# Kernel tuning notes

Measured on AMD Instinct MI355X. Metric: run time of the kernel, lower is better.

## Reference

```python
import jax, jax.numpy as jnp
import numpy as np

B, D, N, K, T = 8192, 256, 2048, 512, 8
M_MARGIN = 1.0
LAMBDA_ORTHO = 1e-3
EPS = 1e-10


def _l2(a, b):
    # squared L2 distance along last axis
    return jnp.sum((a - b) ** 2, axis=-1)


def setup_inputs() -> dict:
    key = jax.random.key(0)
    k1, k2, k3, k4, k5 = jax.random.split(key, 5)
    return {
        "v": jax.random.normal(k1, (B, D), dtype=jnp.float32),
        "vhat": jax.random.normal(k2, (B, D), dtype=jnp.float32),
        "g": jax.random.uniform(k3, (B, K), dtype=jnp.float32),
        "F": jax.random.normal(k4, (K, D), dtype=jnp.float32),
        "negatives": jax.random.normal(k5, (N, D), dtype=jnp.float32),
        "mask": jnp.ones((B,), dtype=bool),
    }


def reference(v, vhat, g, F, negatives, mask):
    maskf = mask.astype(v.dtype)
    msum = maskf.sum()

    # ---- contrastive loss (vectorized over the N-negatives loop) ----
    true_dist = _l2(vhat, v)                                   # [B]
    neg_dist = _l2(vhat[:, None, :], negatives[None, :, :])    # [B, N]
    per = jnp.maximum(1.0 + true_dist[:, None] - neg_dist, 0.0)
    ju_per = per.mean(axis=1) * maskf                          # [B]
    Ju = jnp.where(msum == 0, 0.0, ju_per.sum() / msum)

    # ---- focal triplet loss (topk smallest g, gather F rows) ----
    _, idx = jax.lax.top_k(-g, T)                              # [B, T] indices of t smallest
    g_tz = jnp.take_along_axis(g, idx, axis=1)                 # [B, T]
    F_t = F[idx]                                               # [B, T, D]
    g_t = g_tz / (g_tz.sum(axis=1, keepdims=True) + EPS)
    m_t = M_MARGIN * (1.0 - g_t) ** 2                          # [B, T]
    d_neg = _l2(vhat[:, None, :], F_t)                         # [B, T]
    cur = jnp.maximum(m_t + true_dist[:, None] - d_neg, 0.0)
    jt_per = cur.sum(axis=1) * maskf
    Jt = jnp.where(msum == 0, 0.0, jt_per.sum() / msum)

    # ---- orthogonality regularizer: ||F F^T - I||_F, then squared ----
    gram = F @ F.T - jnp.eye(K, dtype=F.dtype)
    ortho = jnp.sqrt(jnp.sum(gram ** 2))

    Jz = Ju + Jt + LAMBDA_ORTHO * ortho ** 2
    return Jz
```

## Files before the change

### kernel.cpp

```cpp
#include <hip/hip_runtime.h>

#define B_N 8192
#define D_N 256
#define N_N 2048
#define K_N 512
#define T_N 8

using short8  = __attribute__((ext_vector_type(8))) short;
using floatx4 = __attribute__((ext_vector_type(4))) float;


__device__ __forceinline__ float wave_reduce_sum(float x) {
  #pragma unroll
  for (int off = 32; off > 0; off >>= 1) x += __shfl_down(x, off, 64);
  return x;
}

__device__ __forceinline__ unsigned int f2bf(float x) {
  unsigned u = __float_as_uint(x);
  return (u + 0x7fffu + ((u >> 16) & 1u)) >> 16;
}

__device__ __forceinline__ unsigned int pack2bf(float x, float y) {
  return f2bf(x) | (f2bf(y) << 16);
}

__device__ __forceinline__ void gload16(const unsigned short* g, unsigned short* l) {
  __builtin_amdgcn_global_load_lds(
      (const __attribute__((address_space(1))) unsigned int*)g,
      (__attribute__((address_space(3))) unsigned int*)l, 16, 0, 0);
}

#define CSWAP(a, b)                                              \
  {                                                              \
    bool sw_ = sv[a] > sv[b];                                    \
    float tv_ = sw_ ? sv[a] : sv[b];                             \
    sv[a] = sw_ ? sv[b] : sv[a];                                 \
    sv[b] = tv_;                                                 \
    int ti_ = sw_ ? si[a] : si[b];                               \
    si[a] = sw_ ? si[b] : si[a];                                 \
    si[b] = ti_;                                                 \
  }

__global__ __launch_bounds__(256) void prep_kernel(
    const float* __restrict__ v, const float* __restrict__ vhat,
    const float* __restrict__ neg, const float* __restrict__ F,
    const float* __restrict__ g,
    unsigned short* __restrict__ vhat_bf, unsigned short* __restrict__ neg_bf,
    unsigned short* __restrict__ F_bf,
    float* __restrict__ td, float* __restrict__ vn2, float* __restrict__ cb,
    float* __restrict__ nn2, float* __restrict__ fn2,
    float* __restrict__ selc, int* __restrict__ seli) {
  int lane = threadIdx.x & 63;
  int row = (blockIdx.x << 2) + (threadIdx.x >> 6);
  if (row < B_N) {
    const float4 a = *(const float4*)(vhat + (size_t)row * D_N + lane * 4);
    const float4 b = *(const float4*)(v + (size_t)row * D_N + lane * 4);
    float dx = a.x - b.x, dy = a.y - b.y, dz = a.z - b.z, dw = a.w - b.w;
    float t = dx * dx + dy * dy + dz * dz + dw * dw;
    float n = a.x * a.x + a.y * a.y + a.z * a.z + a.w * a.w;
    uint2 p;
    p.x = pack2bf(a.x, a.y);
    p.y = pack2bf(a.z, a.w);
    *(uint2*)(vhat_bf + (size_t)row * D_N + lane * 4) = p;
    t = wave_reduce_sum(t);
    n = wave_reduce_sum(n);
    if (lane == 0) {
      td[row] = t;
      vn2[row] = n;
      cb[row] = 1.0f + t - n;
    }
    const float* grow = g + (size_t)row * K_N;
    float sv[8];
    int si[8];
    {
      float4 g0 = *(const float4*)(grow + lane * 8);
      float4 g1 = *(const float4*)(grow + lane * 8 + 4);
      sv[0] = g0.x; sv[1] = g0.y; sv[2] = g0.z; sv[3] = g0.w;
      sv[4] = g1.x; sv[5] = g1.y; sv[6] = g1.z; sv[7] = g1.w;
      #pragma unroll
      for (int j = 0; j < 8; ++j) si[j] = lane * 8 + j;
    }
    CSWAP(0,1) CSWAP(2,3) CSWAP(4,5) CSWAP(6,7)
    CSWAP(0,2) CSWAP(1,3) CSWAP(4,6) CSWAP(5,7)
    CSWAP(1,2) CSWAP(5,6)
    CSWAP(0,4) CSWAP(1,5) CSWAP(2,6) CSWAP(3,7)
    CSWAP(2,4) CSWAP(3,5)
    CSWAP(1,2) CSWAP(3,4) CSWAP(5,6)
    #pragma unroll
    for (int rr = 0; rr < 6; ++rr) {
      const int msk = 1 << rr;
      float pv[8];
      int pi[8];
      #pragma unroll
      for (int j = 0; j < 8; ++j) {
        pv[j] = __shfl_xor(sv[j], msk, 64);
        pi[j] = __shfl_xor(si[j], msk, 64);
      }
      float cv[8];
      int ci[8];
      #pragma unroll
      for (int j = 0; j < 8; ++j) {
        bool mine = sv[j] <= pv[7 - j];
        cv[j] = mine ? sv[j] : pv[7 - j];
        ci[j] = mine ? si[j] : pi[7 - j];
      }
      #pragma unroll
      for (int j = 0; j < 8; ++j) { sv[j] = cv[j]; si[j] = ci[j]; }
      CSWAP(0,4) CSWAP(1,5) CSWAP(2,6) CSWAP(3,7)
      CSWAP(0,2) CSWAP(1,3) CSWAP(4,6) CSWAP(5,7)
      CSWAP(0,1) CSWAP(2,3) CSWAP(4,5) CSWAP(6,7)
    }
    float gsum = 1e-10f;
    #pragma unroll
    for (int t8 = 0; t8 < T_N; ++t8) gsum += sv[t8];
    if (lane == 0) {
      float base = t - n;
      #pragma unroll
      for (int t8 = 0; t8 < T_N; ++t8) {
        float gt = sv[t8] / gsum;
        float mt = (1.0f - gt) * (1.0f - gt);
        selc[(size_t)row * T_N + t8] = mt + base;
        seli[(size_t)row * T_N + t8] = si[t8];
      }
    }
  } else if (row < B_N + N_N) {
    int r = row - B_N;
    const float4 a = *(const float4*)(neg + (size_t)r * D_N + lane * 4);
    float n = a.x * a.x + a.y * a.y + a.z * a.z + a.w * a.w;
    uint2 p;
    p.x = pack2bf(a.x, a.y);
    p.y = pack2bf(a.z, a.w);
    *(uint2*)(neg_bf + (size_t)r * D_N + lane * 4) = p;
    n = wave_reduce_sum(n);
    if (lane == 0) nn2[r] = n;
  } else {
    int r = row - (B_N + N_N);
    const float4 a = *(const float4*)(F + (size_t)r * D_N + lane * 4);
    float n = a.x * a.x + a.y * a.y + a.z * a.z + a.w * a.w;
    uint2 p;
    p.x = pack2bf(a.x, a.y);
    p.y = pack2bf(a.z, a.w);
    *(uint2*)(F_bf + (size_t)r * D_N + lane * 4) = p;
    n = wave_reduce_sum(n);
    if (lane == 0) fn2[r] = n;
  }
}

__global__ __launch_bounds__(256) void main_kernel(
    const unsigned short* __restrict__ vhat_bf, const unsigned short* __restrict__ neg_bf,
    const unsigned short* __restrict__ F_bf,
    const float* __restrict__ cb, const float* __restrict__ nn2,
    const float* __restrict__ fn2, const int* __restrict__ mask,
    float* __restrict__ ju_part, float* __restrict__ or_part,
    float* __restrict__ W) {
  __shared__ __align__(16) unsigned char smem[16384];
  const int bx = blockIdx.x;
  const int tid = threadIdx.x;
  const int lane = tid & 63;
  const int wave = tid >> 6;

  unsigned short* AsU = (unsigned short*)smem;
  unsigned short* BsU = AsU + 4096;
  int r0, c0;
  const unsigned short *Abase, *Bbase;
  int seg;
  if (bx < 1024) {
    seg = 0;
    r0 = (bx >> 4) * 128;
    c0 = (bx & 15) * 128;
    Abase = vhat_bf;
    Bbase = neg_bf;
  } else if (bx < 1040) {
    seg = 1;
    int o = bx - 1024;
    r0 = (o >> 2) * 128;
    c0 = (o & 3) * 128;
    Abase = F_bf;
    Bbase = F_bf;
  } else {
    seg = 2;
    int o = bx - 1040;
    r0 = (o >> 2) * 128;
    c0 = (o & 3) * 128;
    Abase = vhat_bf;
    Bbase = F_bf;
  }
  const int wx = wave & 1, wy = wave >> 1;

  const int c_slot = lane & 3;
  const int rA0 = wave * 32 + (lane >> 2);
  const int rA1 = rA0 + 16;
  const int cg0 = c_slot ^ ((rA0 >> 1) & 3);
  const int cg1 = c_slot ^ ((rA1 >> 1) & 3);
  const unsigned short* gA0 = Abase + (size_t)(r0 + rA0) * D_N + cg0 * 8;
  const unsigned short* gA1 = Abase + (size_t)(r0 + rA1) * D_N + cg1 * 8;
  const unsigned short* gB0 = Bbase + (size_t)(c0 + rA0) * D_N + cg0 * 8;
  const unsigned short* gB1 = Bbase + (size_t)(c0 + rA1) * D_N + cg1 * 8;
  unsigned short* lA0 = AsU + wave * 1024 + lane * 8;
  unsigned short* lA1 = lA0 + 512;
  unsigned short* lB0 = BsU + wave * 1024 + lane * 8;
  unsigned short* lB1 = lB0 + 512;

  const int fr = lane & 15;
  const int fc = lane >> 4;
  int aoff[4], boff[4];
  #pragma unroll
  for (int i = 0; i < 4; ++i) {
    int ra = wy * 64 + i * 16 + fr;
    aoff[i] = ra * 32 + (fc ^ ((ra >> 1) & 3)) * 8;
    int rb = wx * 64 + i * 16 + fr;
    boff[i] = rb * 32 + (fc ^ ((rb >> 1) & 3)) * 8;
  }

  floatx4 acc[4][4];
  #pragma unroll
  for (int i = 0; i < 4; ++i)
    #pragma unroll
    for (int j = 0; j < 4; ++j)
      acc[i][j] = floatx4{0.0f, 0.0f, 0.0f, 0.0f};

  for (int k0 = 0; k0 < D_N; k0 += 32) {
    __syncthreads();
    gload16(gA0 + k0, lA0);
    gload16(gA1 + k0, lA1);
    gload16(gB0 + k0, lB0);
    gload16(gB1 + k0, lB1);
    __syncthreads();
    short8 af[4], bf[4];
    #pragma unroll
    for (int i = 0; i < 4; ++i) af[i] = *(const short8*)(AsU + aoff[i]);
    #pragma unroll
    for (int j = 0; j < 4; ++j) bf[j] = *(const short8*)(BsU + boff[j]);
    #pragma unroll
    for (int i = 0; i < 4; ++i)
      #pragma unroll
      for (int j = 0; j < 4; ++j)
        acc[i][j] = __builtin_amdgcn_mfma_f32_16x16x32_bf16(af[i], bf[j], acc[i][j], 0, 0, 0);
  }

  if (seg == 0) {
    float nns[4];
    #pragma unroll
    for (int j = 0; j < 4; ++j)
      nns[j] = nn2[c0 + wx * 64 + j * 16 + (lane & 15)];
    float lsum = 0.0f;
    #pragma unroll
    for (int i = 0; i < 4; ++i) {
      #pragma unroll
      for (int r = 0; r < 4; ++r) {
        int b = r0 + wy * 64 + i * 16 + (lane >> 4) * 4 + r;
        float cbb = cb[b];
        float mf = (mask[b] != 0) ? 1.0f : 0.0f;
        float rs = 0.0f;
        #pragma unroll
        for (int j = 0; j < 4; ++j) {
          float val = cbb + 2.0f * acc[i][j][r] - nns[j];
          rs += fmaxf(val, 0.0f);
        }
        lsum += mf * rs;
      }
    }
    lsum = wave_reduce_sum(lsum);
    if (lane == 0) ju_part[bx * 4 + wave] = lsum;
  } else if (seg == 1) {
    float lsum = 0.0f;
    #pragma unroll
    for (int i = 0; i < 4; ++i) {
      #pragma unroll
      for (int r = 0; r < 4; ++r) {
        int gi = r0 + wy * 64 + i * 16 + (lane >> 4) * 4 + r;
        #pragma unroll
        for (int j = 0; j < 4; ++j) {
          int gj = c0 + wx * 64 + j * 16 + (lane & 15);
          float s = (gi == gj) ? (fn2[gi] - 1.0f) : acc[i][j][r];
          lsum += s * s;
        }
      }
    }
    lsum = wave_reduce_sum(lsum);
    if (lane == 0) or_part[(bx - 1024) * 4 + wave] = lsum;
  } else {
    #pragma unroll
    for (int i = 0; i < 4; ++i) {
      #pragma unroll
      for (int r = 0; r < 4; ++r) {
        int row = r0 + wy * 64 + i * 16 + (lane >> 4) * 4 + r;
        #pragma unroll
        for (int j = 0; j < 4; ++j) {
          int col = c0 + wx * 64 + j * 16 + (lane & 15);
          W[(size_t)row * K_N + col] = acc[i][j][r];
        }
      }
    }
  }
}

__global__ __launch_bounds__(256) void jt_gather_kernel(
    const int* __restrict__ seli, const float* __restrict__ selc,
    const float* __restrict__ W, const float* __restrict__ fn2,
    const int* __restrict__ mask, float* __restrict__ jt_part) {
  int b = blockIdx.x * 256 + threadIdx.x;
  int4 i0 = *(const int4*)(seli + (size_t)b * 8);
  int4 i1 = *(const int4*)(seli + (size_t)b * 8 + 4);
  float4 c0 = *(const float4*)(selc + (size_t)b * 8);
  float4 c1 = *(const float4*)(selc + (size_t)b * 8 + 4);
  const float* wrow = W + (size_t)b * K_N;
  float s = 0.0f;
  s += fmaxf(c0.x + 2.0f * wrow[i0.x] - fn2[i0.x], 0.0f);
  s += fmaxf(c0.y + 2.0f * wrow[i0.y] - fn2[i0.y], 0.0f);
  s += fmaxf(c0.z + 2.0f * wrow[i0.z] - fn2[i0.z], 0.0f);
  s += fmaxf(c0.w + 2.0f * wrow[i0.w] - fn2[i0.w], 0.0f);
  s += fmaxf(c1.x + 2.0f * wrow[i1.x] - fn2[i1.x], 0.0f);
  s += fmaxf(c1.y + 2.0f * wrow[i1.y] - fn2[i1.y], 0.0f);
  s += fmaxf(c1.z + 2.0f * wrow[i1.z] - fn2[i1.z], 0.0f);
  s += fmaxf(c1.w + 2.0f * wrow[i1.w] - fn2[i1.w], 0.0f);
  s *= (mask[b] != 0) ? 1.0f : 0.0f;
  s = wave_reduce_sum(s);
  __shared__ float red[4];
  if ((threadIdx.x & 63) == 0) red[threadIdx.x >> 6] = s;
  __syncthreads();
  if (threadIdx.x == 0)
    jt_part[blockIdx.x] = red[0] + red[1] + red[2] + red[3];
}

__global__ __launch_bounds__(256) void finalize_kernel(
    const float* __restrict__ jt_part, const float* __restrict__ ju_part,
    const float* __restrict__ or_part, const int* __restrict__ mask,
    float* __restrict__ out) {
  int tid = threadIdx.x;
  float sjt = 0.0f, sju = 0.0f, sor = 0.0f, sm = 0.0f;
  for (int i = tid; i < B_N; i += 256) sm += (mask[i] != 0) ? 1.0f : 0.0f;
  for (int i = tid; i < 4096; i += 256) sju += ju_part[i];
  if (tid < 64) sor = or_part[tid];
  if (tid < 32) sjt = jt_part[tid];
  sjt = wave_reduce_sum(sjt);
  sju = wave_reduce_sum(sju);
  sor = wave_reduce_sum(sor);
  sm  = wave_reduce_sum(sm);
  __shared__ float red[4][4];
  int lane = tid & 63, w = tid >> 6;
  if (lane == 0) {
    red[w][0] = sjt; red[w][1] = sju; red[w][2] = sor; red[w][3] = sm;
  }
  __syncthreads();
  if (tid == 0) {
    float jt = red[0][0] + red[1][0] + red[2][0] + red[3][0];
    float ju = red[0][1] + red[1][1] + red[2][1] + red[3][1];
    float oo = red[0][2] + red[1][2] + red[2][2] + red[3][2];
    float ms = red[0][3] + red[1][3] + red[2][3] + red[3][3];
    float Ju = (ms == 0.0f) ? 0.0f : ju / ((float)N_N * ms);
    float Jt = (ms == 0.0f) ? 0.0f : jt / ms;
    out[0] = Ju + Jt + 1.0e-3f * oo;
  }
}

extern "C" void kernel_launch(void* const* d_in, const int* in_sizes, int n_in,
                              void* d_out, int out_size, void* d_ws, size_t ws_size,
                              hipStream_t stream) {
  (void)in_sizes; (void)n_in; (void)out_size; (void)ws_size;
  const float* v    = (const float*)d_in[0];
  const float* vhat = (const float*)d_in[1];
  const float* g    = (const float*)d_in[2];
  const float* F    = (const float*)d_in[3];
  const float* neg  = (const float*)d_in[4];
  const int*   mask = (const int*)d_in[5];

  float* ws = (float*)d_ws;
  float* W       = ws;
  float* td      = ws + 4194304;
  float* vn2     = ws + 4202496;
  float* cb      = ws + 4210688;
  float* nn2     = ws + 4218880;
  float* fn2     = ws + 4220928;
  float* ju_part = ws + 4221440;
  float* or_part = ws + 4225536;
  float* jt_part = ws + 4225600;
  float* selc    = ws + 4225632;
  int*   seli    = (int*)(ws + 4291168);
  unsigned short* vhat_bf = (unsigned short*)(ws + 4356704);
  unsigned short* neg_bf  = vhat_bf + (size_t)B_N * D_N;
  unsigned short* F_bf    = neg_bf + (size_t)N_N * D_N;

  prep_kernel<<<(B_N + N_N + K_N) / 4, 256, 0, stream>>>(
      v, vhat, neg, F, g, vhat_bf, neg_bf, F_bf, td, vn2, cb, nn2, fn2,
      selc, seli);
  main_kernel<<<1024 + 16 + 256, 256, 0, stream>>>(
      vhat_bf, neg_bf, F_bf, cb, nn2, fn2, mask, ju_part, or_part, W);
  jt_gather_kernel<<<B_N / 256, 256, 0, stream>>>(
      seli, selc, W, fn2, mask, jt_part);
  finalize_kernel<<<1, 256, 0, stream>>>(jt_part, ju_part, or_part, mask,
                                         (float*)d_out);
}
```

Measured before the change: 126.3 us.

## Fuse focal-triplet gather into GEMM epilogue, drop W matrix round-trip

The vhat·F^T GEMM blocks no longer write the full 8192x512 fp32 W matrix to global memory. Each block stages 16-row slices of its accumulator tile in shared memory and evaluates the hinge terms for the selected top-k indices that fall in its column range, writing per-wave partial sums. This removes a 16 MB write and a separate gather kernel launch. The cost is extra __syncthreads in the epilogue and a larger partial-sum array for the finalize kernel to reduce.

```diff
diff --git a/kernel.cpp b/kernel.cpp
--- a/kernel.cpp
+++ b/kernel.cpp
@@ -152,8 +152,9 @@
     const unsigned short* __restrict__ F_bf,
     const float* __restrict__ cb, const float* __restrict__ nn2,
     const float* __restrict__ fn2, const int* __restrict__ mask,
+    const float* __restrict__ selc, const int* __restrict__ seli,
     float* __restrict__ ju_part, float* __restrict__ or_part,
-    float* __restrict__ W) {
+    float* __restrict__ jt_part) {
   __shared__ __align__(16) unsigned char smem[16384];
   const int bx = blockIdx.x;
   const int tid = threadIdx.x;
@@ -281,47 +282,35 @@
     lsum = wave_reduce_sum(lsum);
     if (lane == 0) or_part[(bx - 1024) * 4 + wave] = lsum;
   } else {
+    float* Wt = (float*)smem;
+    const int quad = lane >> 4, col15 = lane & 15;
+    const int rl = tid >> 3;
+    const int t8 = tid & 7;
+    float jts = 0.0f;
     #pragma unroll
     for (int i = 0; i < 4; ++i) {
+      __syncthreads();
       #pragma unroll
       for (int r = 0; r < 4; ++r) {
-        int row = r0 + wy * 64 + i * 16 + (lane >> 4) * 4 + r;
+        int row_local = wy * 16 + quad * 4 + r;
         #pragma unroll
-        for (int j = 0; j < 4; ++j) {
-          int col = c0 + wx * 64 + j * 16 + (lane & 15);
-          W[(size_t)row * K_N + col] = acc[i][j][r];
-        }
-      }
-    }
-  }
-}
-
-__global__ __launch_bounds__(256) void jt_gather_kernel(
-    const int* __restrict__ seli, const float* __restrict__ selc,
-    const float* __restrict__ W, const float* __restrict__ fn2,
-    const int* __restrict__ mask, float* __restrict__ jt_part) {
-  int b = blockIdx.x * 256 + threadIdx.x;
-  int4 i0 = *(const int4*)(seli + (size_t)b * 8);
-  int4 i1 = *(const int4*)(seli + (size_t)b * 8 + 4);
-  float4 c0 = *(const float4*)(selc + (size_t)b * 8);
-  float4 c1 = *(const float4*)(selc + (size_t)b * 8 + 4);
-  const float* wrow = W + (size_t)b * K_N;
-  float s = 0.0f;
-  s += fmaxf(c0.x + 2.0f * wrow[i0.x] - fn2[i0.x], 0.0f);
-  s += fmaxf(c0.y + 2.0f * wrow[i0.y] - fn2[i0.y], 0.0f);
-  s += fmaxf(c0.z + 2.0f * wrow[i0.z] - fn2[i0.z], 0.0f);
-  s += fmaxf(c0.w + 2.0f * wrow[i0.w] - fn2[i0.w], 0.0f);
-  s += fmaxf(c1.x + 2.0f * wrow[i1.x] - fn2[i1.x], 0.0f);
-  s += fmaxf(c1.y + 2.0f * wrow[i1.y] - fn2[i1.y], 0.0f);
-  s += fmaxf(c1.z + 2.0f * wrow[i1.z] - fn2[i1.z], 0.0f);
-  s += fmaxf(c1.w + 2.0f * wrow[i1.w] - fn2[i1.w], 0.0f);
-  s *= (mask[b] != 0) ? 1.0f : 0.0f;
-  s = wave_reduce_sum(s);
-  __shared__ float red[4];
-  if ((threadIdx.x & 63) == 0) red[threadIdx.x >> 6] = s;
-  __syncthreads();
-  if (threadIdx.x == 0)
-    jt_part[blockIdx.x] = red[0] + red[1] + red[2] + red[3];
+        for (int j = 0; j < 4; ++j)
+          Wt[row_local * 128 + wx * 64 + j * 16 + col15] = acc[i][j][r];
+      }
+      __syncthreads();
+      int b = r0 + (rl & 15) + i * 16 + (rl >> 4) * 64;
+      int idx = seli[(size_t)b * 8 + t8];
+      int c = idx - c0;
+      if ((unsigned)c < 128u) {
+        float w = Wt[rl * 128 + c];
+        float term = selc[(size_t)b * 8 + t8] + 2.0f * w - fn2[idx];
+        float mf = (mask[b] != 0) ? 1.0f : 0.0f;
+        jts += mf * fmaxf(term, 0.0f);
+      }
+    }
+    jts = wave_reduce_sum(jts);
+    if (lane == 0) jt_part[(bx - 1040) * 4 + wave] = jts;
+  }
 }
 
 __global__ __launch_bounds__(256) void finalize_kernel(
@@ -332,8 +321,8 @@
   float sjt = 0.0f, sju = 0.0f, sor = 0.0f, sm = 0.0f;
   for (int i = tid; i < B_N; i += 256) sm += (mask[i] != 0) ? 1.0f : 0.0f;
   for (int i = tid; i < 4096; i += 256) sju += ju_part[i];
+  for (int i = tid; i < 1024; i += 256) sjt += jt_part[i];
   if (tid < 64) sor = or_part[tid];
-  if (tid < 32) sjt = jt_part[tid];
   sjt = wave_reduce_sum(sjt);
   sju = wave_reduce_sum(sju);
   sor = wave_reduce_sum(sor);
@@ -367,18 +356,17 @@
   const int*   mask = (const int*)d_in[5];
 
   float* ws = (float*)d_ws;
-  float* W       = ws;
-  float* td      = ws + 4194304;
-  float* vn2     = ws + 4202496;
-  float* cb      = ws + 4210688;
-  float* nn2     = ws + 4218880;
-  float* fn2     = ws + 4220928;
-  float* ju_part = ws + 4221440;
-  float* or_part = ws + 4225536;
-  float* jt_part = ws + 4225600;
-  float* selc    = ws + 4225632;
-  int*   seli    = (int*)(ws + 4291168);
-  unsigned short* vhat_bf = (unsigned short*)(ws + 4356704);
+  float* td      = ws;
+  float* vn2     = ws + 8192;
+  float* cb      = ws + 16384;
+  float* nn2     = ws + 24576;
+  float* fn2     = ws + 26624;
+  float* ju_part = ws + 27136;
+  float* or_part = ws + 31232;
+  float* jt_part = ws + 31296;
+  float* selc    = ws + 32320;
+  int*   seli    = (int*)(ws + 97856);
+  unsigned short* vhat_bf = (unsigned short*)(ws + 163392);
   unsigned short* neg_bf  = vhat_bf + (size_t)B_N * D_N;
   unsigned short* F_bf    = neg_bf + (size_t)N_N * D_N;
 
@@ -386,9 +374,8 @@
       v, vhat, neg, F, g, vhat_bf, neg_bf, F_bf, td, vn2, cb, nn2, fn2,
       selc, seli);
   main_kernel<<<1024 + 16 + 256, 256, 0, stream>>>(
-      vhat_bf, neg_bf, F_bf, cb, nn2, fn2, mask, ju_part, or_part, W);
-  jt_gather_kernel<<<B_N / 256, 256, 0, stream>>>(
-      seli, selc, W, fn2, mask, jt_part);
+      vhat_bf, neg_bf, F_bf, cb, nn2, fn2, mask, selc, seli,
+      ju_part, or_part, jt_part);
   finalize_kernel<<<1, 256, 0, stream>>>(jt_part, ju_part, or_part, mask,
                                          (float*)d_out);
 }
```

New measurement: 119.3 us. 5.6% less time.
